# Optimization experiments

Hardware: AMD Instinct MI355X
Metric: run time of the kernel (lower is better)

Reference implementation:

```python
import jax, jax.numpy as jnp
import numpy as np

B, S, C, V, LAT, NL = 256, 512, 256, 32, 256, 7
DILS = [1, 2, 4, 8, 16, 32, 64]
EPS = 1e-5


def setup_inputs() -> dict:
    key = jax.random.key(0)
    ks = jax.random.split(key, 24)
    s = 0.05
    inp = {
        "x": jax.random.randint(ks[0], (B, S), 0, V, dtype=jnp.int64 if jax.config.read("jax_enable_x64") else jnp.int32),
        "z": jax.random.normal(ks[1], (B, LAT), dtype=jnp.float32),
        "emb": jax.random.normal(ks[2], (V, C), dtype=jnp.float32) * s,
        "latent_W": jax.random.normal(ks[3], (LAT, C), dtype=jnp.float32) * s,
        "latent_b": jnp.zeros((C,), jnp.float32),
        "ln1_g": jnp.ones((NL, C), jnp.float32),
        "ln1_b": jnp.zeros((NL, C), jnp.float32),
        "w1": jax.random.normal(ks[4], (NL, C, C), jnp.float32) * s,
        "b1": jnp.zeros((NL, C), jnp.float32),
        "ln2_g": jnp.ones((NL, C), jnp.float32),
        "ln2_b": jnp.zeros((NL, C), jnp.float32),
        "wd": jax.random.normal(ks[5], (NL, 2, C, C), jnp.float32) * s,  # tap 0 = x[t-d], tap 1 = x[t]
        "bd": jnp.zeros((NL, C), jnp.float32),
        "ln3_g": jnp.ones((NL, C), jnp.float32),
        "ln3_b": jnp.zeros((NL, C), jnp.float32),
        "we": jax.random.normal(ks[6], (NL, C, C), jnp.float32) * s,
        "be": jnp.zeros((NL, C), jnp.float32),
        "wg": jax.random.normal(ks[7], (NL, C, C), jnp.float32) * s,
        "bg": jnp.zeros((NL, C), jnp.float32),
        "out_W": jax.random.normal(ks[8], (C, V), jnp.float32) * s,
        "out_b": jnp.zeros((V,), jnp.float32),
    }
    return inp


def _ln(h, g, b):
    mu = h.mean(-1, keepdims=True)
    var = jnp.mean((h - mu) ** 2, axis=-1, keepdims=True)
    return (h - mu) * jax.lax.rsqrt(var + EPS) * g + b


def _lrelu(h):
    return jnp.where(h >= 0, h, 0.01 * h)


def reference(x, z, emb, latent_W, latent_b, ln1_g, ln1_b, w1, b1,
              ln2_g, ln2_b, wd, bd, ln3_g, ln3_b, we, be, wg, bg,
              out_W, out_b):
    # channel-last layout [B, S, C] throughout (fuses away the torch transposes)
    h = emb[x] + (z @ latent_W + latent_b)[:, None, :]
    for i, d in enumerate(DILS):
        x_inp = h
        t = _lrelu(_ln(x_inp, ln1_g[i], ln1_b[i]))
        t = t @ w1[i] + b1[i]
        t = _lrelu(_ln(t, ln2_g[i], ln2_b[i]))
        # causal dilated conv, kernel=2: out[t] = W0*x[t-d] + W1*x[t]
        t_shift = jnp.pad(t, ((0, 0), (d, 0), (0, 0)))[:, :t.shape[1], :]
        t = t_shift @ wd[i, 0] + t @ wd[i, 1] + bd[i]
        t = _lrelu(_ln(t, ln3_g[i], ln3_b[i]))
        gated = (t @ we[i] + be[i]) * jax.nn.sigmoid(t @ wg[i] + bg[i])
        h = gated + x_inp
    logits = h @ out_W + out_b                      # [B, S, V]
    lp = jax.nn.log_softmax(logits, axis=-1)
    # gather log-prob of next token: lp[:, :-1, :] at x[:, 1:]
    return jnp.take_along_axis(lp[:, :-1, :], x[:, 1:, None], axis=2)[..., 0]
```

## Files before the change

kernel.cpp:

```cpp
#include <hip/hip_runtime.h>

typedef unsigned short u16;
typedef unsigned int   u32;
typedef __attribute__((ext_vector_type(8))) short short8;
typedef __attribute__((ext_vector_type(4))) float f32x4;

struct __align__(8) u16x4 { u16 x, y, z, w; };

#define NL 7
#define M_DIM 131072

__device__ __forceinline__ float b2f(u16 u) {
  union { float f; u32 i; } c; c.i = ((u32)u) << 16; return c.f;
}
__device__ __forceinline__ u16 f2b(float f) {
  union { float f; u32 i; } c; c.f = f;
  u32 r = c.i + 0x7FFFu + ((c.i >> 16) & 1u);
  return (u16)(r >> 16);
}
__device__ __forceinline__ void gload16(const void* g, void* l) {
  __builtin_amdgcn_global_load_lds((const __attribute__((address_space(1))) void*)g,
                                   (__attribute__((address_space(3))) void*)l, 16, 0, 0);
}
__device__ __forceinline__ int xIdx(int row, int chunk) {
  return row * 256 + (((chunk) ^ (row & 7)) << 3);
}


__global__ __launch_bounds__(256) void conv_w1_k(const float* __restrict__ w1, u16* __restrict__ wT) {
  int idx = blockIdx.x * 256 + threadIdx.x;
  int i = idx >> 16, rem = idx & 65535;
  int n = rem >> 8, k = rem & 255;
  wT[idx] = f2b(w1[(i << 16) + (k << 8) + n]);
}

__global__ __launch_bounds__(256) void conv_wd_k(const float* __restrict__ wd, u16* __restrict__ wT) {
  int idx = blockIdx.x * 256 + threadIdx.x;
  int i = idx / 131072, rem = idx & 131071;
  int n = rem >> 9, k2 = rem & 511;
  int tap = k2 >> 8, k = k2 & 255;
  wT[idx] = f2b(wd[(((i * 2 + tap) << 8) + k) * 256 + n]);
}

__global__ __launch_bounds__(256) void conv_weg_k(const float* __restrict__ we, const float* __restrict__ wg,
                                                  u16* __restrict__ wT) {
  int idx = blockIdx.x * 256 + threadIdx.x;
  int i = idx / 131072, rem = idx & 131071;
  int src = rem >> 16, n = (rem >> 8) & 255, k = rem & 255;
  const float* W = src ? wg : we;
  wT[idx] = f2b(W[((i << 8) + k) * 256 + n]);
}

__global__ __launch_bounds__(256) void conv_wo_k(const float* __restrict__ outW, u16* __restrict__ wTo) {
  int idx = blockIdx.x * 256 + threadIdx.x;
  int v = idx >> 8, k = idx & 255;
  wTo[idx] = f2b(outW[k * 32 + v]);
}


__global__ __launch_bounds__(256) void zlat_k(const float* __restrict__ z, const float* __restrict__ W,
                                              const float* __restrict__ bias, float* __restrict__ zlat) {
  int b = blockIdx.x, c = threadIdx.x;
  float acc = bias[c];
  for (int l = 0; l < 256; ++l) acc += z[b * 256 + l] * W[l * 256 + c];
  zlat[b * 256 + c] = acc;
}


__global__ __launch_bounds__(256) void embed_k(const int* __restrict__ x, const float* __restrict__ emb,
                                               const float* __restrict__ zlat, u16* __restrict__ h) {
  int wave = threadIdx.x >> 6, lane = threadIdx.x & 63;
  int r = blockIdx.x * 4 + wave;
  int c = lane * 4;
  int tok = x[r];
  int bi = r >> 9;
  float4 ev = *(const float4*)&emb[tok * 256 + c];
  float4 zv = *(const float4*)&zlat[bi * 256 + c];
  u16x4 hb;
  hb.x = f2b(ev.x + zv.x); hb.y = f2b(ev.y + zv.y);
  hb.z = f2b(ev.z + zv.z); hb.w = f2b(ev.w + zv.w);
  *(u16x4*)&h[(long)r * 256 + c] = hb;
}


__global__ __launch_bounds__(256, 3) void gemm1_k(
    const u16* __restrict__ h, const u16* __restrict__ WT,
    const float* __restrict__ ln1g, const float* __restrict__ ln1b,
    const float* __restrict__ bias,
    const float* __restrict__ ln2g, const float* __restrict__ ln2b,
    u16* __restrict__ V)
{
  __shared__ __align__(16) u16 lA[64 * 256];
  __shared__ __align__(16) u16 lB[256 * 32];
  float* pS  = (float*)lB;
  float* pQ  = (float*)(lB + 512);
  float* muA = (float*)(lB + 1024);
  float* rsA = (float*)(lB + 1152);
  const int tid = threadIdx.x;
  const int lane = tid & 63;
  const int wv = tid >> 6;
  const int wc = wv * 64;
  const int m0 = blockIdx.x * 64;
  const int rA = tid >> 2;
  const int cSw = ((((tid & 3) - ((tid >> 3) & 3)) & 3)) * 8;
  const int lr = lane & 15;
  const int quad = lane >> 4;
  const int sw = ((quad + ((lr >> 1) & 3)) & 3) * 8;

  {
    const int half = lane >> 5, l5 = lane & 31;
    float4 ga = *(const float4*)&ln1g[l5 * 8];
    float4 gb = *(const float4*)&ln1g[l5 * 8 + 4];
    float4 ba = *(const float4*)&ln1b[l5 * 8];
    float4 bb = *(const float4*)&ln1b[l5 * 8 + 4];
    #pragma unroll 4
    for (int it = 0; it < 8; ++it) {
      int row = wv * 16 + it * 2 + half;
      uint4 hv = *(const uint4*)(h + (long)(m0 + row) * 256 + l5 * 8);
      float v0 = b2f((u16)(hv.x & 0xffff)), v1 = b2f((u16)(hv.x >> 16));
      float v2 = b2f((u16)(hv.y & 0xffff)), v3 = b2f((u16)(hv.y >> 16));
      float v4 = b2f((u16)(hv.z & 0xffff)), v5 = b2f((u16)(hv.z >> 16));
      float v6 = b2f((u16)(hv.w & 0xffff)), v7 = b2f((u16)(hv.w >> 16));
      float s = v0 + v1 + v2 + v3 + v4 + v5 + v6 + v7;
      float q = v0*v0 + v1*v1 + v2*v2 + v3*v3 + v4*v4 + v5*v5 + v6*v6 + v7*v7;
      #pragma unroll
      for (int o = 1; o < 32; o <<= 1) { s += __shfl_xor(s, o); q += __shfl_xor(q, o); }
      float mu = s * 0.00390625f;
      float var = q * 0.00390625f - mu * mu;
      float rs = rsqrtf(var + 1e-5f);
      float y0 = (v0 - mu) * rs * ga.x + ba.x; y0 = y0 >= 0.f ? y0 : 0.01f * y0;
      float y1 = (v1 - mu) * rs * ga.y + ba.y; y1 = y1 >= 0.f ? y1 : 0.01f * y1;
      float y2 = (v2 - mu) * rs * ga.z + ba.z; y2 = y2 >= 0.f ? y2 : 0.01f * y2;
      float y3 = (v3 - mu) * rs * ga.w + ba.w; y3 = y3 >= 0.f ? y3 : 0.01f * y3;
      float y4 = (v4 - mu) * rs * gb.x + bb.x; y4 = y4 >= 0.f ? y4 : 0.01f * y4;
      float y5 = (v5 - mu) * rs * gb.y + bb.y; y5 = y5 >= 0.f ? y5 : 0.01f * y5;
      float y6 = (v6 - mu) * rs * gb.z + bb.z; y6 = y6 >= 0.f ? y6 : 0.01f * y6;
      float y7 = (v7 - mu) * rs * gb.w + bb.w; y7 = y7 >= 0.f ? y7 : 0.01f * y7;
      uint4 ov;
      ov.x = (u32)f2b(y0) | ((u32)f2b(y1) << 16);
      ov.y = (u32)f2b(y2) | ((u32)f2b(y3) << 16);
      ov.z = (u32)f2b(y4) | ((u32)f2b(y5) << 16);
      ov.w = (u32)f2b(y6) | ((u32)f2b(y7) << 16);
      *(uint4*)&lA[xIdx(row, l5)] = ov;
    }
  }

  f32x4 acc[4][4];
  #pragma unroll
  for (int i = 0; i < 4; ++i)
    #pragma unroll
    for (int j = 0; j < 4; ++j) {
      acc[i][j][0] = 0.f; acc[i][j][1] = 0.f; acc[i][j][2] = 0.f; acc[i][j][3] = 0.f;
    }

  for (int kt = 0; kt < 8; ++kt) {
    const long bofs = (long)rA * 256 + kt * 32 + cSw;
    #pragma unroll
    for (int j = 0; j < 4; ++j)
      gload16(WT + bofs + (long)(64 * j) * 256, &lB[tid * 8 + j * 2048]);
    __syncthreads();

    short8 af[4], bfr[4];
    #pragma unroll
    for (int mt = 0; mt < 4; ++mt)
      af[mt] = *(const short8*)&lA[xIdx(mt * 16 + lr, 4 * kt + quad)];
    #pragma unroll
    for (int nt = 0; nt < 4; ++nt)
      bfr[nt] = *(const short8*)&lB[(wc + nt * 16 + lr) * 32 + sw];
    #pragma unroll
    for (int mt = 0; mt < 4; ++mt)
      #pragma unroll
      for (int nt = 0; nt < 4; ++nt)
        acc[mt][nt] = __builtin_amdgcn_mfma_f32_16x16x32_bf16(af[mt], bfr[nt], acc[mt][nt], 0, 0, 0);
    __syncthreads();
  }

  float biasv[4], gv[4], bv[4];
  #pragma unroll
  for (int nt = 0; nt < 4; ++nt) {
    int n = wc + nt * 16 + lr;
    biasv[nt] = bias[n]; gv[nt] = ln2g[n]; bv[nt] = ln2b[n];
  }
  #pragma unroll
  for (int mt = 0; mt < 4; ++mt)
    #pragma unroll
    for (int r = 0; r < 4; ++r) {
      float s = 0.f, q = 0.f;
      #pragma unroll
      for (int nt = 0; nt < 4; ++nt) {
        float v = acc[mt][nt][r] + biasv[nt];
        acc[mt][nt][r] = v;
        s += v; q += v * v;
      }
      #pragma unroll
      for (int o = 1; o < 16; o <<= 1) { s += __shfl_xor(s, o); q += __shfl_xor(q, o); }
      if (lr == 0) { pS[(mt * 16 + quad * 4 + r) * 4 + wv] = s; pQ[(mt * 16 + quad * 4 + r) * 4 + wv] = q; }
    }
  __syncthreads();
  if (tid < 64) {
    float S = pS[tid * 4 + 0] + pS[tid * 4 + 1] + pS[tid * 4 + 2] + pS[tid * 4 + 3];
    float Q = pQ[tid * 4 + 0] + pQ[tid * 4 + 1] + pQ[tid * 4 + 2] + pQ[tid * 4 + 3];
    float mu = S * 0.00390625f;
    float var = Q * 0.00390625f - mu * mu;
    muA[tid] = mu; rsA[tid] = rsqrtf(var + 1e-5f);
  }
  __syncthreads();
  #pragma unroll
  for (int mt = 0; mt < 4; ++mt)
    #pragma unroll
    for (int r = 0; r < 4; ++r) {
      int row = mt * 16 + quad * 4 + r;
      float mu = muA[row], rs = rsA[row];
      #pragma unroll
      for (int nt = 0; nt < 4; ++nt) {
        float y = (acc[mt][nt][r] - mu) * rs * gv[nt] + bv[nt];
        y = y >= 0.f ? y : 0.01f * y;
        V[(long)(m0 + row) * 256 + wc + nt * 16 + lr] = f2b(y);
      }
    }
}


__global__ __launch_bounds__(256, 3) void conv_gate_k(
    const u16* __restrict__ A,
    const u16* __restrict__ WTd,
    int dil,
    const float* __restrict__ bd3, const float* __restrict__ g3, const float* __restrict__ bb3,
    const u16* __restrict__ WTe, const u16* __restrict__ WTg,
    const float* __restrict__ bev_, const float* __restrict__ bgv_,
    u16* __restrict__ h)
{
  __shared__ __align__(16) u16 pT[64 * 256];
  __shared__ __align__(16) u16 stg[10240];
  float* pS  = (float*)stg;
  float* pQ  = (float*)(stg + 512);
  float* muA = (float*)(stg + 1024);
  float* rsA = (float*)(stg + 1152);
  u16* stgW = stg + 2048;

  const int tid = threadIdx.x;
  const int lane = tid & 63;
  const int wv = tid >> 6;
  const int wc = wv * 64;
  const int m0 = blockIdx.x * 64;
  const int rA = tid >> 2;
  const int cSw = ((((tid & 3) - ((tid >> 3) & 3)) & 3)) * 8;
  const int lr = lane & 15;
  const int quad = lane >> 4;
  const int sw = ((quad + ((lr >> 1) & 3)) & 3) * 8;
  const int mm = m0 + rA;
  const int s1 = mm & 511;
  const short8 zero8 = {0, 0, 0, 0, 0, 0, 0, 0};

  bool zz[4];
  #pragma unroll
  for (int mt = 0; mt < 4; ++mt)
    zz[mt] = ((m0 + mt * 16 + lr) & 511) < dil;

  f32x4 acc[4][4];
  #pragma unroll
  for (int i = 0; i < 4; ++i)
    #pragma unroll
    for (int j = 0; j < 4; ++j) {
      acc[i][j][0] = 0.f; acc[i][j][1] = 0.f; acc[i][j][2] = 0.f; acc[i][j][3] = 0.f;
    }

  for (int kt = 0; kt < 16; ++kt) {
    const int kk = (kt & 7) * 32;
    {
      const int rr = (kt < 8 && s1 >= dil) ? (mm - dil) : mm;
      gload16(A + (long)rr * 256 + kk + cSw, &stg[tid * 8]);
      const u16* bS = WTd + kt * 32 + cSw;
      gload16(bS + (long)rA * 512,         &stgW[tid * 8]);
      gload16(bS + (long)(rA + 64) * 512,  &stgW[tid * 8 + 2048]);
      gload16(bS + (long)(rA + 128) * 512, &stgW[tid * 8 + 4096]);
      gload16(bS + (long)(rA + 192) * 512, &stgW[tid * 8 + 6144]);
    }
    __syncthreads();

    short8 af[4], bfr[4];
    #pragma unroll
    for (int mt = 0; mt < 4; ++mt) {
      af[mt] = *(const short8*)&stg[(mt * 16 + lr) * 32 + sw];
      if (kt < 8 && zz[mt]) af[mt] = zero8;
    }
    #pragma unroll
    for (int nt = 0; nt < 4; ++nt)
      bfr[nt] = *(const short8*)&stgW[(wc + nt * 16 + lr) * 32 + sw];
    #pragma unroll
    for (int mt = 0; mt < 4; ++mt)
      #pragma unroll
      for (int nt = 0; nt < 4; ++nt)
        acc[mt][nt] = __builtin_amdgcn_mfma_f32_16x16x32_bf16(af[mt], bfr[nt], acc[mt][nt], 0, 0, 0);
    __syncthreads();
  }

  {
    const long bofs = (long)rA * 256 + cSw;
    gload16(WTe + bofs,              &stgW[tid * 8]);
    gload16(WTe + bofs + 64L * 256,  &stgW[tid * 8 + 2048]);
    gload16(WTe + bofs + 128L * 256, &stgW[tid * 8 + 4096]);
    gload16(WTe + bofs + 192L * 256, &stgW[tid * 8 + 6144]);
  }

  float b3v[4], g3v[4], o3v[4];
  #pragma unroll
  for (int nt = 0; nt < 4; ++nt) {
    int n = wc + nt * 16 + lr;
    b3v[nt] = bd3[n]; g3v[nt] = g3[n]; o3v[nt] = bb3[n];
  }
  #pragma unroll
  for (int mt = 0; mt < 4; ++mt)
    #pragma unroll
    for (int r = 0; r < 4; ++r) {
      float s = 0.f, q = 0.f;
      #pragma unroll
      for (int nt = 0; nt < 4; ++nt) {
        float v = acc[mt][nt][r] + b3v[nt];
        acc[mt][nt][r] = v;
        s += v; q += v * v;
      }
      #pragma unroll
      for (int o = 1; o < 16; o <<= 1) { s += __shfl_xor(s, o); q += __shfl_xor(q, o); }
      if (lr == 0) { pS[(mt * 16 + quad * 4 + r) * 4 + wv] = s; pQ[(mt * 16 + quad * 4 + r) * 4 + wv] = q; }
    }
  __syncthreads();
  if (tid < 64) {
    float S = pS[tid * 4 + 0] + pS[tid * 4 + 1] + pS[tid * 4 + 2] + pS[tid * 4 + 3];
    float Q = pQ[tid * 4 + 0] + pQ[tid * 4 + 1] + pQ[tid * 4 + 2] + pQ[tid * 4 + 3];
    float mu = S * 0.00390625f;
    float var = Q * 0.00390625f - mu * mu;
    muA[tid] = mu; rsA[tid] = rsqrtf(var + 1e-5f);
  }
  __syncthreads();
  #pragma unroll
  for (int mt = 0; mt < 4; ++mt)
    #pragma unroll
    for (int r = 0; r < 4; ++r) {
      int row = mt * 16 + quad * 4 + r;
      float mu = muA[row], rs = rsA[row];
      #pragma unroll
      for (int nt = 0; nt < 4; ++nt) {
        int col = wc + nt * 16 + lr;
        float y = (acc[mt][nt][r] - mu) * rs * g3v[nt] + o3v[nt];
        y = y >= 0.f ? y : 0.01f * y;
        pT[xIdx(row, col >> 3) + (col & 7)] = f2b(y);
      }
    }
  __syncthreads();

  f32x4 accE[4][4], accG[4][4];
  #pragma unroll
  for (int i = 0; i < 4; ++i)
    #pragma unroll
    for (int j = 0; j < 4; ++j) {
      accE[i][j][0] = 0.f; accE[i][j][1] = 0.f; accE[i][j][2] = 0.f; accE[i][j][3] = 0.f;
      accG[i][j][0] = 0.f; accG[i][j][1] = 0.f; accG[i][j][2] = 0.f; accG[i][j][3] = 0.f;
    }

  for (int kt = 0; kt < 8; ++kt) {
    short8 paf[4], bfe[4];
    #pragma unroll
    for (int mt = 0; mt < 4; ++mt)
      paf[mt] = *(const short8*)&pT[xIdx(mt * 16 + lr, 4 * kt + quad)];
    #pragma unroll
    for (int nt = 0; nt < 4; ++nt)
      bfe[nt] = *(const short8*)&stgW[(wc + nt * 16 + lr) * 32 + sw];
    #pragma unroll
    for (int mt = 0; mt < 4; ++mt)
      #pragma unroll
      for (int nt = 0; nt < 4; ++nt)
        accE[mt][nt] = __builtin_amdgcn_mfma_f32_16x16x32_bf16(paf[mt], bfe[nt], accE[mt][nt], 0, 0, 0);
    __syncthreads();
    if (kt < 7) {
      const long bofs = (long)rA * 256 + (kt + 1) * 32 + cSw;
      gload16(WTe + bofs,              &stgW[tid * 8]);
      gload16(WTe + bofs + 64L * 256,  &stgW[tid * 8 + 2048]);
      gload16(WTe + bofs + 128L * 256, &stgW[tid * 8 + 4096]);
      gload16(WTe + bofs + 192L * 256, &stgW[tid * 8 + 6144]);
    } else {
      const long bofs = (long)rA * 256 + cSw;
      gload16(WTg + bofs,              &stgW[tid * 8]);
      gload16(WTg + bofs + 64L * 256,  &stgW[tid * 8 + 2048]);
      gload16(WTg + bofs + 128L * 256, &stgW[tid * 8 + 4096]);
      gload16(WTg + bofs + 192L * 256, &stgW[tid * 8 + 6144]);
    }
    __syncthreads();
  }

  for (int kt = 0; kt < 8; ++kt) {
    short8 paf[4], bfg[4];
    #pragma unroll
    for (int mt = 0; mt < 4; ++mt)
      paf[mt] = *(const short8*)&pT[xIdx(mt * 16 + lr, 4 * kt + quad)];
    #pragma unroll
    for (int nt = 0; nt < 4; ++nt)
      bfg[nt] = *(const short8*)&stgW[(wc + nt * 16 + lr) * 32 + sw];
    #pragma unroll
    for (int mt = 0; mt < 4; ++mt)
      #pragma unroll
      for (int nt = 0; nt < 4; ++nt)
        accG[mt][nt] = __builtin_amdgcn_mfma_f32_16x16x32_bf16(paf[mt], bfg[nt], accG[mt][nt], 0, 0, 0);
    if (kt < 7) {
      __syncthreads();
      const long bofs = (long)rA * 256 + (kt + 1) * 32 + cSw;
      gload16(WTg + bofs,              &stgW[tid * 8]);
      gload16(WTg + bofs + 64L * 256,  &stgW[tid * 8 + 2048]);
      gload16(WTg + bofs + 128L * 256, &stgW[tid * 8 + 4096]);
      gload16(WTg + bofs + 192L * 256, &stgW[tid * 8 + 6144]);
      __syncthreads();
    }
  }

  float bev[4], bgv[4];
  #pragma unroll
  for (int nt = 0; nt < 4; ++nt) {
    int n = wc + nt * 16 + lr;
    bev[nt] = bev_[n]; bgv[nt] = bgv_[n];
  }
  #pragma unroll
  for (int mt = 0; mt < 4; ++mt)
    #pragma unroll
    for (int r = 0; r < 4; ++r) {
      int row = mt * 16 + quad * 4 + r;
      long off = (long)(m0 + row) * 256;
      #pragma unroll
      for (int nt = 0; nt < 4; ++nt) {
        int n = wc + nt * 16 + lr;
        float e = accE[mt][nt][r] + bev[nt];
        float gg = accG[mt][nt][r] + bgv[nt];
        float hn = e * (1.f / (1.f + expf(-gg))) + b2f(h[off + n]);
        h[off + n] = f2b(hn);
      }
    }
}


__global__ __launch_bounds__(256) void final_k(const u16* __restrict__ h, const u16* __restrict__ WTo,
                                               const float* __restrict__ outb, const int* __restrict__ x,
                                               float* __restrict__ out) {
  __shared__ u16 lW[32 * 264];
  const int tid = threadIdx.x;
  const int lane = tid & 63;
  const int wv = tid >> 6;
  const int mBase = blockIdx.x * 256 + wv * 64;

  #pragma unroll
  for (int j = 0; j < 4; ++j) {
    int chunk = tid + 256 * j;
    int v = chunk >> 5, k8 = chunk & 31;
    uint4 w4 = *(const uint4*)(WTo + v * 256 + k8 * 8);
    *(uint4*)&lW[v * 264 + k8 * 8] = w4;
  }
  __syncthreads();

  const int lq = (lane >> 4) * 8;
  const int lr = lane & 15;
  const int quad = lane >> 4;

  f32x4 acc[4][2];
  #pragma unroll
  for (int mt = 0; mt < 4; ++mt) {
    acc[mt][0][0] = 0.f; acc[mt][0][1] = 0.f; acc[mt][0][2] = 0.f; acc[mt][0][3] = 0.f;
    acc[mt][1][0] = 0.f; acc[mt][1][1] = 0.f; acc[mt][1][2] = 0.f; acc[mt][1][3] = 0.f;
  }

  for (int kt = 0; kt < 8; ++kt) {
    short8 bf0 = *(const short8*)&lW[lr * 264 + kt * 32 + lq];
    short8 bf1 = *(const short8*)&lW[(16 + lr) * 264 + kt * 32 + lq];
    #pragma unroll
    for (int mt = 0; mt < 4; ++mt) {
      short8 af = *(const short8*)(h + (long)(mBase + mt * 16 + lr) * 256 + kt * 32 + lq);
      acc[mt][0] = __builtin_amdgcn_mfma_f32_16x16x32_bf16(af, bf0, acc[mt][0], 0, 0, 0);
      acc[mt][1] = __builtin_amdgcn_mfma_f32_16x16x32_bf16(af, bf1, acc[mt][1], 0, 0, 0);
    }
  }

  float ob0 = outb[lr], ob1 = outb[16 + lr];
  #pragma unroll
  for (int mt = 0; mt < 4; ++mt)
    #pragma unroll
    for (int r = 0; r < 4; ++r) {
      int row = mBase + mt * 16 + quad * 4 + r;
      float lo = acc[mt][0][r] + ob0;
      float hi = acc[mt][1][r] + ob1;
      float mx = fmaxf(lo, hi);
      #pragma unroll
      for (int o = 1; o < 16; o <<= 1) mx = fmaxf(mx, __shfl_xor(mx, o));
      float se = expf(lo - mx) + expf(hi - mx);
      #pragma unroll
      for (int o = 1; o < 16; o <<= 1) se += __shfl_xor(se, o);
      int s = row & 511;
      int xa = (s == 511) ? row : (row + 1);
      int tok = x[xa];
      float lg = (tok < 16) ? lo : hi;
      float lp = lg - mx - logf(se);
      if (s != 511 && lr == (tok & 15))
        out[(row >> 9) * 511 + s] = lp;
    }
}


extern "C" void kernel_launch(void* const* d_in, const int* in_sizes, int n_in,
                              void* d_out, int out_size, void* d_ws, size_t ws_size,
                              hipStream_t stream) {
  const int*   x    = (const int*)d_in[0];
  const float* z    = (const float*)d_in[1];
  const float* emb  = (const float*)d_in[2];
  const float* latW = (const float*)d_in[3];
  const float* latb = (const float*)d_in[4];
  const float* ln1g = (const float*)d_in[5];
  const float* ln1b = (const float*)d_in[6];
  const float* w1   = (const float*)d_in[7];
  const float* b1   = (const float*)d_in[8];
  const float* ln2g = (const float*)d_in[9];
  const float* ln2b = (const float*)d_in[10];
  const float* wd   = (const float*)d_in[11];
  const float* bd   = (const float*)d_in[12];
  const float* ln3g = (const float*)d_in[13];
  const float* ln3b = (const float*)d_in[14];
  const float* we   = (const float*)d_in[15];
  const float* be   = (const float*)d_in[16];
  const float* wg   = (const float*)d_in[17];
  const float* bg   = (const float*)d_in[18];
  const float* outW = (const float*)d_in[19];
  const float* outb = (const float*)d_in[20];

  char* ws = (char*)d_ws;
  u16*   h    = (u16*)(ws + 0);
  u16*   bufA = (u16*)(ws + 67108864);
  float* zlat = (float*)(ws + 201326592);
  u16*   wT1  = (u16*)(ws + 201588736);
  u16*   wTd  = (u16*)(ws + 202506240);
  u16*   wTeg = (u16*)(ws + 204341248);
  u16*   wTo  = (u16*)(ws + 206176256);

  conv_w1_k <<<1792, 256, 0, stream>>>(w1, wT1);
  conv_wd_k <<<3584, 256, 0, stream>>>(wd, wTd);
  conv_weg_k<<<3584, 256, 0, stream>>>(we, wg, wTeg);
  conv_wo_k <<<32, 256, 0, stream>>>(outW, wTo);
  zlat_k    <<<256, 256, 0, stream>>>(z, latW, latb, zlat);
  embed_k   <<<M_DIM / 4, 256, 0, stream>>>(x, emb, zlat, h);

  for (int i = 0; i < NL; ++i) {
    int d = 1 << i;
    gemm1_k<<<M_DIM / 64, 256, 0, stream>>>(
        h, wT1 + i * 65536, ln1g + i * 256, ln1b + i * 256, b1 + i * 256,
        ln2g + i * 256, ln2b + i * 256, bufA);
    conv_gate_k<<<M_DIM / 64, 256, 0, stream>>>(
        bufA, wTd + i * 131072, d,
        bd + i * 256, ln3g + i * 256, ln3b + i * 256,
        wTeg + i * 131072, wTeg + i * 131072 + 65536,
        be + i * 256, bg + i * 256, h);
  }

  final_k<<<M_DIM / 256, 256, 0, stream>>>(h, wTo, outb, x, (float*)d_out);
}
```

Before: 1.468 ms.

## Double-buffer conv_gate staging and widen block to 128 rows with 8 waves

Restructures conv_gate_k to use 512 threads over a 128-row tile, with 8 waves split 2x4 across rows and columns. Each weight tile loaded into LDS is now shared by twice as many rows. Staging buffers are double-buffered, and the next K-slice is prefetched while the current MFMAs run, coordinated by explicit vmcnt/lgkmcnt waits and raw barriers in place of paired __syncthreads. This aims to hide global-load latency and halve per-row weight traffic. In exchange, LDS use per block rises to about 112KB, which limits residency, and the hand-written waitcnt counts must match the number of outstanding loads or data races appear.

```diff
diff --git a/kernel.cpp b/kernel.cpp
--- a/kernel.cpp
+++ b/kernel.cpp
@@ -9,6 +9,10 @@
 
 #define NL 7
 #define M_DIM 131072
+
+#define VMW(N) asm volatile("s_waitcnt vmcnt(" #N ")" ::: "memory")
+#define LGW()  asm volatile("s_waitcnt lgkmcnt(0)" ::: "memory")
+#define BAR()  __builtin_amdgcn_s_barrier()
 
 __device__ __forceinline__ float b2f(u16 u) {
   union { float f; u32 i; } c; c.i = ((u32)u) << 16; return c.f;
@@ -221,7 +225,7 @@
 }
 
 
-__global__ __launch_bounds__(256, 3) void conv_gate_k(
+__global__ __launch_bounds__(512, 2) void conv_gate_k(
     const u16* __restrict__ A,
     const u16* __restrict__ WTd,
     int dil,
@@ -230,19 +234,21 @@
     const float* __restrict__ bev_, const float* __restrict__ bgv_,
     u16* __restrict__ h)
 {
-  __shared__ __align__(16) u16 pT[64 * 256];
-  __shared__ __align__(16) u16 stg[10240];
-  float* pS  = (float*)stg;
-  float* pQ  = (float*)(stg + 512);
-  float* muA = (float*)(stg + 1024);
-  float* rsA = (float*)(stg + 1152);
-  u16* stgW = stg + 2048;
+  __shared__ __align__(16) u16 pT[128 * 256];
+  __shared__ __align__(16) u16 stg[2][12288];
+  float* pS  = (float*)stg[0];
+  float* pQ  = (float*)(stg[0] + 1024);
+  float* muA = (float*)(stg[0] + 2048);
+  float* rsA = (float*)(stg[0] + 2304);
 
   const int tid = threadIdx.x;
   const int lane = tid & 63;
   const int wv = tid >> 6;
-  const int wc = wv * 64;
-  const int m0 = blockIdx.x * 64;
+  const int mw = wv >> 2;
+  const int nw = wv & 3;
+  const int rb = mw * 64;
+  const int wc = nw * 64;
+  const int m0 = blockIdx.x * 128;
   const int rA = tid >> 2;
   const int cSw = ((((tid & 3) - ((tid >> 3) & 3)) & 3)) * 8;
   const int lr = lane & 15;
@@ -255,7 +261,22 @@
   bool zz[4];
   #pragma unroll
   for (int mt = 0; mt < 4; ++mt)
-    zz[mt] = ((m0 + mt * 16 + lr) & 511) < dil;
+    zz[mt] = ((m0 + rb + mt * 16 + lr) & 511) < dil;
+
+#define STAGE1(KT, BB) do {                                                   \
+    const int kt_ = (KT);                                                     \
+    const int kk_ = (kt_ & 7) * 32;                                           \
+    const int rr_ = (kt_ < 8 && s1 >= dil) ? (mm - dil) : mm;                 \
+    gload16(A + (long)rr_ * 256 + kk_ + cSw, &stg[BB][tid * 8]);              \
+    const u16* bS_ = WTd + kt_ * 32 + cSw;                                    \
+    gload16(bS_ + (long)rA * 512,         &stg[BB][4096 + tid * 8]);          \
+    gload16(bS_ + (long)(rA + 128) * 512, &stg[BB][8192 + tid * 8]);          \
+  } while (0)
+#define STAGEW(WP, KT, BB) do {                                               \
+    const long bofs_ = (long)rA * 256 + (KT) * 32 + cSw;                      \
+    gload16((WP) + bofs_,              &stg[BB][4096 + tid * 8]);             \
+    gload16((WP) + bofs_ + 128L * 256, &stg[BB][8192 + tid * 8]);             \
+  } while (0)
 
   f32x4 acc[4][4];
   #pragma unroll
@@ -265,42 +286,36 @@
       acc[i][j][0] = 0.f; acc[i][j][1] = 0.f; acc[i][j][2] = 0.f; acc[i][j][3] = 0.f;
     }
 
-  for (int kt = 0; kt < 16; ++kt) {
-    const int kk = (kt & 7) * 32;
-    {
-      const int rr = (kt < 8 && s1 >= dil) ? (mm - dil) : mm;
-      gload16(A + (long)rr * 256 + kk + cSw, &stg[tid * 8]);
-      const u16* bS = WTd + kt * 32 + cSw;
-      gload16(bS + (long)rA * 512,         &stgW[tid * 8]);
-      gload16(bS + (long)(rA + 64) * 512,  &stgW[tid * 8 + 2048]);
-      gload16(bS + (long)(rA + 128) * 512, &stgW[tid * 8 + 4096]);
-      gload16(bS + (long)(rA + 192) * 512, &stgW[tid * 8 + 6144]);
-    }
-    __syncthreads();
-
+  STAGE1(0, 0);
+  STAGE1(1, 1);
+  VMW(3);
+  BAR();
+
+  #pragma unroll
+  for (int r = 0; r < 16; ++r) {
+    const int bb = r & 1;
     short8 af[4], bfr[4];
     #pragma unroll
     for (int mt = 0; mt < 4; ++mt) {
-      af[mt] = *(const short8*)&stg[(mt * 16 + lr) * 32 + sw];
-      if (kt < 8 && zz[mt]) af[mt] = zero8;
+      af[mt] = *(const short8*)&stg[bb][(rb + mt * 16 + lr) * 32 + sw];
+      if (r < 8 && zz[mt]) af[mt] = zero8;
     }
     #pragma unroll
     for (int nt = 0; nt < 4; ++nt)
-      bfr[nt] = *(const short8*)&stgW[(wc + nt * 16 + lr) * 32 + sw];
+      bfr[nt] = *(const short8*)&stg[bb][4096 + (wc + nt * 16 + lr) * 32 + sw];
+    LGW();
+    BAR();
+    if (r <= 13)      STAGE1(r + 2, bb);
+    else if (r == 14) STAGEW(WTe, 0, 0);
+    else              STAGEW(WTe, 1, 1);
     #pragma unroll
     for (int mt = 0; mt < 4; ++mt)
       #pragma unroll
       for (int nt = 0; nt < 4; ++nt)
         acc[mt][nt] = __builtin_amdgcn_mfma_f32_16x16x32_bf16(af[mt], bfr[nt], acc[mt][nt], 0, 0, 0);
-    __syncthreads();
-  }
-
-  {
-    const long bofs = (long)rA * 256 + cSw;
-    gload16(WTe + bofs,              &stgW[tid * 8]);
-    gload16(WTe + bofs + 64L * 256,  &stgW[tid * 8 + 2048]);
-    gload16(WTe + bofs + 128L * 256, &stgW[tid * 8 + 4096]);
-    gload16(WTe + bofs + 192L * 256, &stgW[tid * 8 + 6144]);
+    if (r <= 13)      VMW(3);
+    else if (r == 14) VMW(2);
+    BAR();
   }
 
   float b3v[4], g3v[4], o3v[4];
@@ -322,22 +337,25 @@
       }
       #pragma unroll
       for (int o = 1; o < 16; o <<= 1) { s += __shfl_xor(s, o); q += __shfl_xor(q, o); }
-      if (lr == 0) { pS[(mt * 16 + quad * 4 + r) * 4 + wv] = s; pQ[(mt * 16 + quad * 4 + r) * 4 + wv] = q; }
-    }
-  __syncthreads();
-  if (tid < 64) {
+      if (lr == 0) {
+        int row = rb + mt * 16 + quad * 4 + r;
+        pS[row * 4 + nw] = s; pQ[row * 4 + nw] = q;
+      }
+    }
+  LGW(); BAR();
+  if (tid < 128) {
     float S = pS[tid * 4 + 0] + pS[tid * 4 + 1] + pS[tid * 4 + 2] + pS[tid * 4 + 3];
     float Q = pQ[tid * 4 + 0] + pQ[tid * 4 + 1] + pQ[tid * 4 + 2] + pQ[tid * 4 + 3];
     float mu = S * 0.00390625f;
     float var = Q * 0.00390625f - mu * mu;
     muA[tid] = mu; rsA[tid] = rsqrtf(var + 1e-5f);
   }
-  __syncthreads();
+  LGW(); BAR();
   #pragma unroll
   for (int mt = 0; mt < 4; ++mt)
     #pragma unroll
     for (int r = 0; r < 4; ++r) {
-      int row = mt * 16 + quad * 4 + r;
+      int row = rb + mt * 16 + quad * 4 + r;
       float mu = muA[row], rs = rsA[row];
       #pragma unroll
       for (int nt = 0; nt < 4; ++nt) {
@@ -347,7 +365,7 @@
         pT[xIdx(row, col >> 3) + (col & 7)] = f2b(y);
       }
     }
-  __syncthreads();
+  LGW(); VMW(2); BAR();
 
   f32x4 accE[4][4], accG[4][4];
   #pragma unroll
@@ -358,58 +376,49 @@
       accG[i][j][0] = 0.f; accG[i][j][1] = 0.f; accG[i][j][2] = 0.f; accG[i][j][3] = 0.f;
     }
 
-  for (int kt = 0; kt < 8; ++kt) {
+  #pragma unroll
+  for (int k = 0; k < 8; ++k) {
+    const int bb = k & 1;
     short8 paf[4], bfe[4];
     #pragma unroll
     for (int mt = 0; mt < 4; ++mt)
-      paf[mt] = *(const short8*)&pT[xIdx(mt * 16 + lr, 4 * kt + quad)];
+      paf[mt] = *(const short8*)&pT[xIdx(rb + mt * 16 + lr, 4 * k + quad)];
     #pragma unroll
     for (int nt = 0; nt < 4; ++nt)
-      bfe[nt] = *(const short8*)&stgW[(wc + nt * 16 + lr) * 32 + sw];
+      bfe[nt] = *(const short8*)&stg[bb][4096 + (wc + nt * 16 + lr) * 32 + sw];
+    LGW(); BAR();
+    if (k <= 5)      STAGEW(WTe, k + 2, bb);
+    else if (k == 6) STAGEW(WTg, 0, 0);
+    else             STAGEW(WTg, 1, 1);
     #pragma unroll
     for (int mt = 0; mt < 4; ++mt)
       #pragma unroll
       for (int nt = 0; nt < 4; ++nt)
         accE[mt][nt] = __builtin_amdgcn_mfma_f32_16x16x32_bf16(paf[mt], bfe[nt], accE[mt][nt], 0, 0, 0);
-    __syncthreads();
-    if (kt < 7) {
-      const long bofs = (long)rA * 256 + (kt + 1) * 32 + cSw;
-      gload16(WTe + bofs,              &stgW[tid * 8]);
-      gload16(WTe + bofs + 64L * 256,  &stgW[tid * 8 + 2048]);
-      gload16(WTe + bofs + 128L * 256, &stgW[tid * 8 + 4096]);
-      gload16(WTe + bofs + 192L * 256, &stgW[tid * 8 + 6144]);
-    } else {
-      const long bofs = (long)rA * 256 + cSw;
-      gload16(WTg + bofs,              &stgW[tid * 8]);
-      gload16(WTg + bofs + 64L * 256,  &stgW[tid * 8 + 2048]);
-      gload16(WTg + bofs + 128L * 256, &stgW[tid * 8 + 4096]);
-      gload16(WTg + bofs + 192L * 256, &stgW[tid * 8 + 6144]);
-    }
-    __syncthreads();
-  }
-
-  for (int kt = 0; kt < 8; ++kt) {
+    VMW(2);
+    BAR();
+  }
+
+  #pragma unroll
+  for (int k = 0; k < 8; ++k) {
+    const int bb = k & 1;
     short8 paf[4], bfg[4];
     #pragma unroll
     for (int mt = 0; mt < 4; ++mt)
-      paf[mt] = *(const short8*)&pT[xIdx(mt * 16 + lr, 4 * kt + quad)];
+      paf[mt] = *(const short8*)&pT[xIdx(rb + mt * 16 + lr, 4 * k + quad)];
     #pragma unroll
     for (int nt = 0; nt < 4; ++nt)
-      bfg[nt] = *(const short8*)&stgW[(wc + nt * 16 + lr) * 32 + sw];
+      bfg[nt] = *(const short8*)&stg[bb][4096 + (wc + nt * 16 + lr) * 32 + sw];
+    LGW(); BAR();
+    if (k <= 5) STAGEW(WTg, k + 2, bb);
     #pragma unroll
     for (int mt = 0; mt < 4; ++mt)
       #pragma unroll
       for (int nt = 0; nt < 4; ++nt)
         accG[mt][nt] = __builtin_amdgcn_mfma_f32_16x16x32_bf16(paf[mt], bfg[nt], accG[mt][nt], 0, 0, 0);
-    if (kt < 7) {
-      __syncthreads();
-      const long bofs = (long)rA * 256 + (kt + 1) * 32 + cSw;
-      gload16(WTg + bofs,              &stgW[tid * 8]);
-      gload16(WTg + bofs + 64L * 256,  &stgW[tid * 8 + 2048]);
-      gload16(WTg + bofs + 128L * 256, &stgW[tid * 8 + 4096]);
-      gload16(WTg + bofs + 192L * 256, &stgW[tid * 8 + 6144]);
-      __syncthreads();
-    }
+    if (k <= 5)      VMW(2);
+    else if (k == 6) VMW(0);
+    if (k <= 6) BAR();
   }
 
   float bev[4], bgv[4];
@@ -422,7 +431,7 @@
   for (int mt = 0; mt < 4; ++mt)
     #pragma unroll
     for (int r = 0; r < 4; ++r) {
-      int row = mt * 16 + quad * 4 + r;
+      int row = rb + mt * 16 + quad * 4 + r;
       long off = (long)(m0 + row) * 256;
       #pragma unroll
       for (int nt = 0; nt < 4; ++nt) {
@@ -433,6 +442,8 @@
         h[off + n] = f2b(hn);
       }
     }
+#undef STAGE1
+#undef STAGEW
 }
 
 
@@ -547,7 +558,7 @@
     gemm1_k<<<M_DIM / 64, 256, 0, stream>>>(
         h, wT1 + i * 65536, ln1g + i * 256, ln1b + i * 256, b1 + i * 256,
         ln2g + i * 256, ln2b + i * 256, bufA);
-    conv_gate_k<<<M_DIM / 64, 256, 0, stream>>>(
+    conv_gate_k<<<M_DIM / 128, 512, 0, stream>>>(
         bufA, wTd + i * 131072, d,
         bd + i * 256, ln3g + i * 256, ln3b + i * 256,
         wTeg + i * 131072, wTeg + i * 131072 + 65536,
```

Result: faster. 1.411 ms (-3.9%).
